# Optimization experiments

Measured on AMD Instinct MI355X. Metric: run time of the kernel, lower is better.

Reference implementation:

```python
import jax, jax.numpy as jnp
import numpy as np

N = 4096        # n_locations
D_MODEL = 512
H, D_K, D_V = 4, 128, 256


def setup_inputs() -> dict:
    key = jax.random.key(0)
    ks = jax.random.split(key, 7)
    s = 0.02
    return {
        "Q": jax.random.normal(ks[0], (N, D_MODEL), dtype=jnp.float32),
        "K": jax.random.normal(ks[1], (N, D_MODEL), dtype=jnp.float32),
        "V": jax.random.normal(ks[2], (N, D_MODEL), dtype=jnp.float32),
        "Wq": jax.random.normal(ks[3], (H, D_MODEL, D_K), dtype=jnp.float32) * s,
        "Wk": jax.random.normal(ks[4], (H, D_MODEL, D_K), dtype=jnp.float32) * s,
        "Wv": jax.random.normal(ks[5], (H, D_MODEL, D_V), dtype=jnp.float32) * s,
        "Wo": jax.random.normal(ks[6], (D_MODEL, H * D_V), dtype=jnp.float32) * s,
    }


def reference(Q, K, V, Wq, Wk, Wv, Wo):
    n = K.shape[0]
    # Batched per-head projections: [h, n, d_k] / [h, n, d_v]
    q = jnp.einsum('nd,hdk->hnk', Q, Wq)
    k = jnp.einsum('nd,hdk->hnk', K, Wk)
    v = jnp.einsum('nd,hdv->hnv', V, Wv)
    # NOTE: original scales by sqrt(n_locations) (K.size(0)), not sqrt(d_k)
    scores = jnp.einsum('hqk,hnk->hqn', q, k) / jnp.sqrt(jnp.asarray(n, q.dtype))
    weights = jax.nn.softmax(scores, axis=-1)          # [h, n, n]
    heads = jnp.einsum('hqn,hnv->hqv', weights, v)      # [h, n, d_v]
    # concat heads along feature dim: [n, h*d_v]
    x = jnp.transpose(heads, (1, 0, 2)).reshape(heads.shape[1], -1)
    return x @ Wo.T                                     # [n, d_model]
```

## Files before the change

kernel.cpp:

```cpp
#include <hip/hip_runtime.h>
#include <hip/hip_bf16.h>
#include <type_traits>

typedef __hip_bfloat16 bf16;
typedef __attribute__((ext_vector_type(8))) short bf16x8;
typedef __attribute__((ext_vector_type(4))) float f32x4;

#define N_LOC 4096

__device__ __forceinline__ bf16 to_bf16(float f) { return __float2bfloat16(f); }

__device__ __forceinline__ void dma16(const bf16* g, bf16* l) {
  __builtin_amdgcn_global_load_lds((const __attribute__((address_space(1))) unsigned int*)g,
                                   (__attribute__((address_space(3))) unsigned int*)l, 16, 0, 0);
}

__global__ __launch_bounds__(256) void convert_all(const float* __restrict__ Q,
                                                   const float* __restrict__ K,
                                                   const float* __restrict__ V,
                                                   const float* __restrict__ Wo,
                                                   bf16* __restrict__ Qb, bf16* __restrict__ Kb,
                                                   bf16* __restrict__ Vb, bf16* __restrict__ Wob) {
  long i = ((long)blockIdx.x * 256 + threadIdx.x) * 8;
  const float* src;
  bf16* dst;
  long off;
  if (i < 2097152)      { src = Q;  dst = Qb;  off = i; }
  else if (i < 4194304) { src = K;  dst = Kb;  off = i - 2097152; }
  else if (i < 6291456) { src = V;  dst = Vb;  off = i - 4194304; }
  else                  { src = Wo; dst = Wob; off = i - 6291456; }
  float4 a = *(const float4*)&src[off];
  float4 b = *(const float4*)&src[off + 4];
  union { bf16 h[8]; bf16x8 v; } u;
  u.h[0] = to_bf16(a.x); u.h[1] = to_bf16(a.y); u.h[2] = to_bf16(a.z); u.h[3] = to_bf16(a.w);
  u.h[4] = to_bf16(b.x); u.h[5] = to_bf16(b.y); u.h[6] = to_bf16(b.z); u.h[7] = to_bf16(b.w);
  *(bf16x8*)&dst[off] = u.v;
}

__global__ __launch_bounds__(256) void pack_wt(const float* __restrict__ Wq,
                                               const float* __restrict__ Wk,
                                               const float* __restrict__ Wv,
                                               bf16* __restrict__ oq, bf16* __restrict__ ok,
                                               bf16* __restrict__ ov) {
  int z = blockIdx.z;
  const float* W = (z == 0) ? Wq : (z == 1) ? Wk : Wv;
  bf16* out = (z == 0) ? oq : (z == 1) ? ok : ov;
  int DH = (z == 2) ? 256 : 128;
  int nt = DH >> 6;
  int y = blockIdx.y;
  if (y >= 4 * nt) return;
  int h = y / nt, tt = y - h * nt;
  int d0 = blockIdx.x * 64, t0 = tt * 64;
  __shared__ float tile[64][65];
  for (int i = threadIdx.x; i < 4096; i += 256) {
    int r = i >> 6, c = i & 63;
    tile[r][c] = W[((size_t)h * 512 + d0 + r) * DH + t0 + c];
  }
  __syncthreads();
  for (int i = threadIdx.x; i < 4096; i += 256) {
    int t = i >> 6, d = i & 63;
    out[((size_t)(h * DH + t0 + t)) * 512 + d0 + d] = to_bf16(tile[d][t]);
  }
}

template <typename OutT>
__device__ __forceinline__ void gemm128_body(const bf16* __restrict__ A,
                                             const bf16* __restrict__ Bt,
                                             OutT* __restrict__ C, int M, int N, int K,
                                             int m0, int n0, bf16* As, bf16* Bs) {
  int tid = threadIdx.x;
  int lane = tid & 63, w = tid >> 6;
  int quad = lane >> 4, l16 = lane & 15;
  int wm = (w >> 1) * 64, wn = (w & 1) * 64;
  int srow = lane >> 3;
  int sG = (lane & 7) ^ srow;

  f32x4 acc[4][4] = {};
  for (int k0 = 0; k0 < K; k0 += 64) {
#pragma unroll
    for (int j = 0; j < 4; j++) {
      int rg = 4 * j + w;
      dma16(&A[(long)(m0 + rg * 8 + srow) * K + k0 + sG * 8], &As[rg * 512]);
      dma16(&Bt[(long)(n0 + rg * 8 + srow) * K + k0 + sG * 8], &Bs[rg * 512]);
    }
    __syncthreads();
#pragma unroll
    for (int kk = 0; kk < 2; kk++) {
      bf16x8 af[4], bfr[4];
#pragma unroll
      for (int i = 0; i < 4; i++) {
        int r = wm + i * 16 + l16;
        af[i] = *(const bf16x8*)&As[r * 64 + (((kk * 4 + quad) ^ r) & 7) * 8];
      }
#pragma unroll
      for (int j = 0; j < 4; j++) {
        int r = wn + j * 16 + l16;
        bfr[j] = *(const bf16x8*)&Bs[r * 64 + (((kk * 4 + quad) ^ r) & 7) * 8];
      }
#pragma unroll
      for (int i = 0; i < 4; i++)
#pragma unroll
        for (int j = 0; j < 4; j++)
          acc[i][j] = __builtin_amdgcn_mfma_f32_16x16x32_bf16(af[i], bfr[j], acc[i][j], 0, 0, 0);
    }
    __syncthreads();
  }
#pragma unroll
  for (int i = 0; i < 4; i++)
#pragma unroll
    for (int j = 0; j < 4; j++)
#pragma unroll
      for (int r = 0; r < 4; r++) {
        long row = m0 + wm + i * 16 + quad * 4 + r;
        long col = n0 + wn + j * 16 + l16;
        if constexpr (std::is_same<OutT, bf16>::value)
          C[row * N + col] = to_bf16(acc[i][j][r]);
        else
          C[row * N + col] = acc[i][j][r];
      }
}

__global__ __launch_bounds__(256) void proj_gemm(const bf16* __restrict__ QKVb,
                                                 const bf16* __restrict__ Wt,
                                                 bf16* __restrict__ Cout) {
  int z = blockIdx.z;
  int N = (z == 2) ? 1024 : 512;
  if ((int)(blockIdx.y * 128) >= N) return;
  __shared__ __align__(16) bf16 As[128 * 64];
  __shared__ __align__(16) bf16 Bs[128 * 64];
  const bf16* A = QKVb + (size_t)z * 2097152;
  const bf16* Bt = Wt + ((z == 2) ? (size_t)524288 : (size_t)z * 262144);
  bf16* C = Cout + (size_t)z * 2097152;
  gemm128_body<bf16>(A, Bt, C, 4096, N, 512, blockIdx.x * 128, blockIdx.y * 128, As, Bs);
}

__global__ __launch_bounds__(256) void out_gemm(const bf16* __restrict__ xin,
                                                const bf16* __restrict__ Wob,
                                                float* __restrict__ outp) {
  __shared__ __align__(16) bf16 As[128 * 64];
  __shared__ __align__(16) bf16 Bs[128 * 64];
  gemm128_body<float>(xin, Wob, outp, 4096, 512, 1024, blockIdx.x * 128, blockIdx.y * 128, As, Bs);
}

__global__ __launch_bounds__(256) void transpose_bf16(const bf16* __restrict__ in,
                                                      bf16* __restrict__ out, int R, int Cc) {
  long T = (long)blockIdx.x * 256 + threadIdx.x;
  long nrb = (long)(R >> 3);
  long rb = T % nrb;
  long cb = T / nrb;
  union { bf16 h[8]; bf16x8 v; } a[8], b[8];
#pragma unroll
  for (int i = 0; i < 8; i++) a[i].v = *(const bf16x8*)&in[(rb * 8 + i) * Cc + cb * 8];
#pragma unroll
  for (int j = 0; j < 8; j++) {
#pragma unroll
    for (int i = 0; i < 8; i++) b[j].h[i] = a[i].h[j];
    *(bf16x8*)&out[(cb * 8 + j) * R + rb * 8] = b[j].v;
  }
}

__global__ __launch_bounds__(512, 2) void attn(const bf16* __restrict__ qb,
                                               const bf16* __restrict__ kb,
                                               const bf16* __restrict__ vT,
                                               bf16* __restrict__ x) {
  __shared__ __align__(16) bf16 kt[2][64 * 128];
  __shared__ __align__(16) bf16 vt[2][256 * 64];
  __shared__ __align__(16) bf16 pt[64 * 72];
  __shared__ float Lrow[64];

  const int head = blockIdx.x & 3;
  const int q0 = (blockIdx.x >> 2) * 64;
  const int tid = threadIdx.x;
  const int lane = tid & 63, w = tid >> 6;
  const int quad = lane >> 4, l16 = lane & 15;
  const int cd = w & 3;
  const int g = w >> 2;

  bf16x8 onesf;
  {
    union { bf16 h[8]; bf16x8 v; } u;
    bf16 one = to_bf16(1.0f), zero = to_bf16(0.0f);
#pragma unroll
    for (int j = 0; j < 8; j++) u.h[j] = (l16 == 0) ? one : zero;
    onesf = u.v;
  }

  bf16x8 qf[2][4];
#pragma unroll
  for (int i = 0; i < 2; i++) {
    const bf16* qrow = &qb[(size_t)(q0 + g * 32 + i * 16 + l16) * 512 + head * 128];
#pragma unroll
    for (int kk = 0; kk < 4; kk++) qf[i][kk] = *(const bf16x8*)&qrow[kk * 32 + quad * 8];
  }

  f32x4 oacc[2][4] = {};
  f32x4 oL[2] = {};
  const float scale = 1.0f / 64.0f;

  auto stage = [&](int b, int key0) {
#pragma unroll
    for (int t2 = 0; t2 < 2; t2++) {
      int j = 2 * w + t2;
      int r = 4 * j + (lane >> 4);
      int p = lane & 15;
      int G = (p & 8) | ((p ^ r) & 7);
      dma16(&kb[(size_t)(key0 + r) * 512 + head * 128 + G * 8], &kt[b][j * 512]);
    }
#pragma unroll
    for (int t2 = 0; t2 < 4; t2++) {
      int j = 4 * w + t2;
      int r = 8 * j + (lane >> 3);
      int p = lane & 7;
      int G = (p ^ r) & 7;
      dma16(&vT[(size_t)(head * 256 + r) * 4096 + key0 + G * 8], &vt[b][j * 512]);
    }
  };

  stage(0, 0);
  asm volatile("" ::: "memory");
  int cur = 0;

  for (int t = 0; t < 64; ++t) {
    if (t < 63) {
      stage(cur ^ 1, (t + 1) * 64);
      asm volatile("s_waitcnt vmcnt(6)" ::: "memory");
    } else {
      asm volatile("s_waitcnt vmcnt(0)" ::: "memory");
    }
    __builtin_amdgcn_s_barrier();
    asm volatile("" ::: "memory");

    const bf16* ktc = kt[cur];
    f32x4 sacc[2] = {};
#pragma unroll
    for (int kk = 0; kk < 4; kk++) {
      int R = cd * 16 + l16;
      int G = kk * 4 + quad;
      bf16x8 kf = *(const bf16x8*)&ktc[R * 128 + (((G ^ R) & 7) | (G & 8)) * 8];
      sacc[0] = __builtin_amdgcn_mfma_f32_16x16x32_bf16(qf[0][kk], kf, sacc[0], 0, 0, 0);
      sacc[1] = __builtin_amdgcn_mfma_f32_16x16x32_bf16(qf[1][kk], kf, sacc[1], 0, 0, 0);
    }
#pragma unroll
    for (int i = 0; i < 2; i++)
#pragma unroll
      for (int r = 0; r < 4; r++)
        pt[(g * 32 + i * 16 + quad * 4 + r) * 72 + cd * 16 + l16] =
            to_bf16(__expf(sacc[i][r] * scale));
    asm volatile("s_waitcnt lgkmcnt(0)" ::: "memory");
    __builtin_amdgcn_s_barrier();
    asm volatile("" ::: "memory");

    const bf16* vtc = vt[cur];
#pragma unroll
    for (int kk = 0; kk < 2; kk++) {
      bf16x8 pf[2];
#pragma unroll
      for (int i = 0; i < 2; i++)
        pf[i] = *(const bf16x8*)&pt[(g * 32 + i * 16 + l16) * 72 + kk * 32 + quad * 8];
#pragma unroll
      for (int c = 0; c < 4; c++) {
        int R = cd * 64 + c * 16 + l16;
        int G = kk * 4 + quad;
        bf16x8 vf = *(const bf16x8*)&vtc[R * 64 + ((G ^ R) & 7) * 8];
#pragma unroll
        for (int i = 0; i < 2; i++)
          oacc[i][c] = __builtin_amdgcn_mfma_f32_16x16x32_bf16(pf[i], vf, oacc[i][c], 0, 0, 0);
      }
      if (cd == 3) {
#pragma unroll
        for (int i = 0; i < 2; i++)
          oL[i] = __builtin_amdgcn_mfma_f32_16x16x32_bf16(pf[i], onesf, oL[i], 0, 0, 0);
      }
    }
    asm volatile("" ::: "memory");
    __builtin_amdgcn_s_barrier();
    asm volatile("" ::: "memory");
    cur ^= 1;
  }

  if (cd == 3 && l16 == 0) {
#pragma unroll
    for (int i = 0; i < 2; i++)
#pragma unroll
      for (int r = 0; r < 4; r++) Lrow[g * 32 + i * 16 + quad * 4 + r] = oL[i][r];
  }
  __syncthreads();

#pragma unroll
  for (int i = 0; i < 2; i++)
#pragma unroll
    for (int c = 0; c < 4; c++)
#pragma unroll
      for (int r = 0; r < 4; r++) {
        int row = g * 32 + i * 16 + quad * 4 + r;
        float v = oacc[i][c][r] / Lrow[row];
        x[(size_t)(q0 + row) * 1024 + head * 256 + cd * 64 + c * 16 + l16] = to_bf16(v);
      }
}

extern "C" void kernel_launch(void* const* d_in, const int* in_sizes, int n_in,
                              void* d_out, int out_size, void* d_ws, size_t ws_size,
                              hipStream_t stream) {
  const float* Q  = (const float*)d_in[0];
  const float* Km = (const float*)d_in[1];
  const float* V  = (const float*)d_in[2];
  const float* Wq = (const float*)d_in[3];
  const float* Wk = (const float*)d_in[4];
  const float* Wv = (const float*)d_in[5];
  const float* Wo = (const float*)d_in[6];
  float* out = (float*)d_out;

  bf16* ws  = (bf16*)d_ws;
  bf16* Qb  = ws;
  bf16* Kb  = Qb + 2097152;
  bf16* Vb  = Kb + 2097152;
  bf16* Wqt = Vb + 2097152;
  bf16* Wkt = Wqt + 262144;
  bf16* Wvt = Wkt + 262144;
  bf16* Wob = Wvt + 524288;
  bf16* qb  = Wob + 524288;
  bf16* kb  = qb + 2097152;
  bf16* vb  = kb + 2097152;
  bf16* vT  = vb + 4194304;
  bf16* x   = vT + 4194304;

  convert_all<<<3328, 256, 0, stream>>>(Q, Km, V, Wo, Qb, Kb, Vb, Wob);
  pack_wt<<<dim3(8, 16, 3), 256, 0, stream>>>(Wq, Wk, Wv, Wqt, Wkt, Wvt);

  proj_gemm<<<dim3(32, 8, 3), 256, 0, stream>>>(Qb, Wqt, qb);
  transpose_bf16<<<256, 256, 0, stream>>>(vb, vT, 4096, 1024);

  attn<<<256, 512, 0, stream>>>(qb, kb, vT, x);

  out_gemm<<<dim3(32, 4), 256, 0, stream>>>(x, Wob, out);
}
```

Measured before the change: 227.8 us.

## Triple-buffer attention K/V tiles, drop trailing barrier, and add XCD-aware block mapping

The attention kernel moves from double to triple buffering of K/V tiles, prefetching two tiles ahead and issuing the next stage after the barrier. That lets the end-of-iteration barrier be removed. Blocks are remapped so each XCD works on a single head, which should improve L2 reuse of K/V, and s_setprio raises wave priority around the MFMA sections. The output GEMM switches to 128x64 tiles with twice as many blocks to fill more CUs. The cost is more LDS per block, which may lower occupancy against the launch bound of two blocks per CU.

```diff
diff --git a/kernel.cpp b/kernel.cpp
--- a/kernel.cpp
+++ b/kernel.cpp
@@ -63,44 +63,47 @@
   }
 }
 
-template <typename OutT>
-__device__ __forceinline__ void gemm128_body(const bf16* __restrict__ A,
-                                             const bf16* __restrict__ Bt,
-                                             OutT* __restrict__ C, int M, int N, int K,
-                                             int m0, int n0, bf16* As, bf16* Bs) {
+template <int BN, typename OutT>
+__device__ __forceinline__ void gemm_body(const bf16* __restrict__ A,
+                                          const bf16* __restrict__ Bt,
+                                          OutT* __restrict__ C, int N, int K,
+                                          int m0, int n0, bf16* As, bf16* Bs) {
+  constexpr int WN = BN / 2;
+  constexpr int JN = WN / 16;
   int tid = threadIdx.x;
   int lane = tid & 63, w = tid >> 6;
   int quad = lane >> 4, l16 = lane & 15;
-  int wm = (w >> 1) * 64, wn = (w & 1) * 64;
+  int wm = (w >> 1) * 64, wn = (w & 1) * WN;
   int srow = lane >> 3;
   int sG = (lane & 7) ^ srow;
 
-  f32x4 acc[4][4] = {};
+  f32x4 acc[4][JN] = {};
   for (int k0 = 0; k0 < K; k0 += 64) {
 #pragma unroll
     for (int j = 0; j < 4; j++) {
       int rg = 4 * j + w;
       dma16(&A[(long)(m0 + rg * 8 + srow) * K + k0 + sG * 8], &As[rg * 512]);
-      dma16(&Bt[(long)(n0 + rg * 8 + srow) * K + k0 + sG * 8], &Bs[rg * 512]);
+      if (j < BN / 32)
+        dma16(&Bt[(long)(n0 + rg * 8 + srow) * K + k0 + sG * 8], &Bs[rg * 512]);
     }
     __syncthreads();
 #pragma unroll
     for (int kk = 0; kk < 2; kk++) {
-      bf16x8 af[4], bfr[4];
+      bf16x8 af[4], bfr[JN];
 #pragma unroll
       for (int i = 0; i < 4; i++) {
         int r = wm + i * 16 + l16;
         af[i] = *(const bf16x8*)&As[r * 64 + (((kk * 4 + quad) ^ r) & 7) * 8];
       }
 #pragma unroll
-      for (int j = 0; j < 4; j++) {
+      for (int j = 0; j < JN; j++) {
         int r = wn + j * 16 + l16;
         bfr[j] = *(const bf16x8*)&Bs[r * 64 + (((kk * 4 + quad) ^ r) & 7) * 8];
       }
 #pragma unroll
       for (int i = 0; i < 4; i++)
 #pragma unroll
-        for (int j = 0; j < 4; j++)
+        for (int j = 0; j < JN; j++)
           acc[i][j] = __builtin_amdgcn_mfma_f32_16x16x32_bf16(af[i], bfr[j], acc[i][j], 0, 0, 0);
     }
     __syncthreads();
@@ -108,7 +111,7 @@
 #pragma unroll
   for (int i = 0; i < 4; i++)
 #pragma unroll
-    for (int j = 0; j < 4; j++)
+    for (int j = 0; j < JN; j++)
 #pragma unroll
       for (int r = 0; r < 4; r++) {
         long row = m0 + wm + i * 16 + quad * 4 + r;
@@ -131,15 +134,15 @@
   const bf16* A = QKVb + (size_t)z * 2097152;
   const bf16* Bt = Wt + ((z == 2) ? (size_t)524288 : (size_t)z * 262144);
   bf16* C = Cout + (size_t)z * 2097152;
-  gemm128_body<bf16>(A, Bt, C, 4096, N, 512, blockIdx.x * 128, blockIdx.y * 128, As, Bs);
+  gemm_body<128, bf16>(A, Bt, C, N, 512, blockIdx.x * 128, blockIdx.y * 128, As, Bs);
 }
 
 __global__ __launch_bounds__(256) void out_gemm(const bf16* __restrict__ xin,
                                                 const bf16* __restrict__ Wob,
                                                 float* __restrict__ outp) {
   __shared__ __align__(16) bf16 As[128 * 64];
-  __shared__ __align__(16) bf16 Bs[128 * 64];
-  gemm128_body<float>(xin, Wob, outp, 4096, 512, 1024, blockIdx.x * 128, blockIdx.y * 128, As, Bs);
+  __shared__ __align__(16) bf16 Bs[64 * 64];
+  gemm_body<64, float>(xin, Wob, outp, 512, 1024, blockIdx.x * 128, blockIdx.y * 64, As, Bs);
 }
 
 __global__ __launch_bounds__(256) void transpose_bf16(const bf16* __restrict__ in,
@@ -163,13 +166,15 @@
                                                const bf16* __restrict__ kb,
                                                const bf16* __restrict__ vT,
                                                bf16* __restrict__ x) {
-  __shared__ __align__(16) bf16 kt[2][64 * 128];
-  __shared__ __align__(16) bf16 vt[2][256 * 64];
+  __shared__ __align__(16) bf16 kt[3][64 * 128];
+  __shared__ __align__(16) bf16 vt[3][256 * 64];
   __shared__ __align__(16) bf16 pt[64 * 72];
   __shared__ float Lrow[64];
 
-  const int head = blockIdx.x & 3;
-  const int q0 = (blockIdx.x >> 2) * 64;
+  const int bid = blockIdx.x;
+  const int xcd = bid & 7;
+  const int head = xcd & 3;
+  const int q0 = ((xcd >> 2) * 32 + (bid >> 3)) * 64;
   const int tid = threadIdx.x;
   const int lane = tid & 63, w = tid >> 6;
   const int quad = lane >> 4, l16 = lane & 15;
@@ -217,21 +222,24 @@
   };
 
   stage(0, 0);
+  stage(1, 64);
   asm volatile("" ::: "memory");
-  int cur = 0;
+  int bc = 0;
 
   for (int t = 0; t < 64; ++t) {
-    if (t < 63) {
-      stage(cur ^ 1, (t + 1) * 64);
-      asm volatile("s_waitcnt vmcnt(6)" ::: "memory");
-    } else {
-      asm volatile("s_waitcnt vmcnt(0)" ::: "memory");
-    }
+    if (t < 63) asm volatile("s_waitcnt vmcnt(6)" ::: "memory");
+    else        asm volatile("s_waitcnt vmcnt(0)" ::: "memory");
     __builtin_amdgcn_s_barrier();
     asm volatile("" ::: "memory");
 
-    const bf16* ktc = kt[cur];
+    if (t < 62) {
+      int bs = bc + 2; if (bs >= 3) bs -= 3;
+      stage(bs, (t + 2) * 64);
+    }
+
+    const bf16* ktc = kt[bc];
     f32x4 sacc[2] = {};
+    __builtin_amdgcn_s_setprio(1);
 #pragma unroll
     for (int kk = 0; kk < 4; kk++) {
       int R = cd * 16 + l16;
@@ -240,6 +248,7 @@
       sacc[0] = __builtin_amdgcn_mfma_f32_16x16x32_bf16(qf[0][kk], kf, sacc[0], 0, 0, 0);
       sacc[1] = __builtin_amdgcn_mfma_f32_16x16x32_bf16(qf[1][kk], kf, sacc[1], 0, 0, 0);
     }
+    __builtin_amdgcn_s_setprio(0);
 #pragma unroll
     for (int i = 0; i < 2; i++)
 #pragma unroll
@@ -250,7 +259,8 @@
     __builtin_amdgcn_s_barrier();
     asm volatile("" ::: "memory");
 
-    const bf16* vtc = vt[cur];
+    const bf16* vtc = vt[bc];
+    __builtin_amdgcn_s_setprio(1);
 #pragma unroll
     for (int kk = 0; kk < 2; kk++) {
       bf16x8 pf[2];
@@ -272,10 +282,9 @@
           oL[i] = __builtin_amdgcn_mfma_f32_16x16x32_bf16(pf[i], onesf, oL[i], 0, 0, 0);
       }
     }
+    __builtin_amdgcn_s_setprio(0);
     asm volatile("" ::: "memory");
-    __builtin_amdgcn_s_barrier();
-    asm volatile("" ::: "memory");
-    cur ^= 1;
+    bc = (bc + 1 == 3) ? 0 : bc + 1;
   }
 
   if (cd == 3 && l16 == 0) {
@@ -332,5 +341,5 @@
 
   attn<<<256, 512, 0, stream>>>(qb, kb, vT, x);
 
-  out_gemm<<<dim3(32, 4), 256, 0, stream>>>(x, Wob, out);
-}
+  out_gemm<<<dim3(32, 8), 256, 0, stream>>>(x, Wob, out);
+}
```

Measured after the change: 220.8 us. -3.1%, faster.
